# Kernel tuning notes

Hardware: AMD Instinct MI355X
Metric: run time of the kernel (lower is better)

Reference implementation:

```python
import jax, jax.numpy as jnp
import numpy as np

N_QUBITS = 8
N_CYCLES = 4
N_LAYERS = 2  # log2(8) - 1
B = 65536

CNOT = jnp.array([[1, 0, 0, 0],
                  [0, 1, 0, 0],
                  [0, 0, 0, 1],
                  [0, 0, 1, 0]], dtype=jnp.complex64)


def apply_gate(state, U, wires):
    """Apply a (2^k x 2^k) gate U on the given wires of state (B, 2,2,...,2).
    Wire 0 is the leftmost (most significant) qubit axis."""
    k = len(wires)
    src = [w + 1 for w in wires]
    dst = list(range(1, 1 + k))
    st = jnp.moveaxis(state, src, dst)
    shp = st.shape
    st = st.reshape(shp[0], 2 ** k, -1)
    st = jnp.einsum('ij,bjr->bir', U, st)
    return jnp.moveaxis(st.reshape(shp), dst, src)


def apply_ry(state, q, angles):
    """Batched RY(angle) on qubit q; angles has shape (B,)."""
    st = jnp.moveaxis(state, q + 1, 1)  # (B, 2, rest...)
    c = jnp.cos(0.5 * angles).reshape((-1,) + (1,) * (st.ndim - 2))
    s = jnp.sin(0.5 * angles).reshape((-1,) + (1,) * (st.ndim - 2))
    s0, s1 = st[:, 0], st[:, 1]
    new = jnp.stack([c * s0 - s * s1, s * s0 + c * s1], axis=1)
    return jnp.moveaxis(new, 1, q + 1)


def crx_mat(theta):
    c = (jnp.cos(0.5 * theta) + 0j).astype(jnp.complex64)
    s = (-1j * jnp.sin(0.5 * theta)).astype(jnp.complex64)
    one = jnp.ones((), jnp.complex64)
    zero = jnp.zeros((), jnp.complex64)
    return jnp.stack([
        jnp.stack([one, zero, zero, zero]),
        jnp.stack([zero, one, zero, zero]),
        jnp.stack([zero, zero, c, s]),
        jnp.stack([zero, zero, s, c]),
    ])


def u3_mat(p):
    th, ph, lm = p[0], p[1], p[2]
    ct = (jnp.cos(0.5 * th) + 0j).astype(jnp.complex64)
    st = (jnp.sin(0.5 * th) + 0j).astype(jnp.complex64)
    el = jnp.exp(1j * lm).astype(jnp.complex64)
    ep = jnp.exp(1j * ph).astype(jnp.complex64)
    return jnp.stack([
        jnp.stack([ct, -el * st]),
        jnp.stack([ep * st, ep * el * ct]),
    ])


def expval_z(state, q):
    st = jnp.moveaxis(state, q + 1, 1)
    p = (st.real ** 2 + st.imag ** 2).reshape(st.shape[0], 2, -1).sum(-1)
    return p[:, 0] - p[:, 1]


def _forward(x, crx_theta, u3_params, w1, b1, w2, b2):
    b = x.shape[0]
    # |0...0> initial state, shape (B, 2,2,...,2)
    state = jnp.zeros((b, 2 ** N_QUBITS), jnp.complex64).at[:, 0].set(1.0)
    state = state.reshape((b,) + (2,) * N_QUBITS)
    # encoder: data re-uploading RY angle encoding + CNOT ring, n_cycles times
    for _ in range(N_CYCLES):
        for q in range(N_QUBITS):
            state = apply_ry(state, q, x[:, q])
        for q in range(N_QUBITS):
            state = apply_gate(state, CNOT, [q, (q + 1) % N_QUBITS])
    # QCNN conv/pool layers with shared weights per layer
    active = list(range(N_QUBITS))
    for layer in range(N_LAYERS):
        U = crx_mat(crx_theta[layer])
        for i in range(0, len(active) - 1, 2):
            state = apply_gate(state, U, [active[i], active[i + 1]])
        for i in range(1, len(active) - 1, 2):
            state = apply_gate(state, U, [active[i], active[i + 1]])
        remain = active[1::2]
        # mid-circuit expval in the original is discarded and does not alter state
        V = u3_mat(u3_params[layer])
        for q in remain:
            state = apply_gate(state, V, [q])
        active = remain
    feats = jnp.stack([expval_z(state, q) for q in active], axis=1)  # (B, 2)
    h = jnp.tanh(feats @ w1 + b1)
    return jax.nn.sigmoid(h @ w2 + b2)  # (B, 1)


def setup_inputs() -> dict:
    key = jax.random.key(0)
    ks = jax.random.split(key, 6)
    return {
        'x': jax.random.normal(ks[0], (B, N_QUBITS), jnp.float32),
        'crx_theta': jax.random.normal(ks[1], (N_LAYERS,), jnp.float32),
        'u3_params': jax.random.normal(ks[2], (N_LAYERS, 3), jnp.float32),
        'w1': jax.random.normal(ks[3], (2, 10), jnp.float32) * 0.5,
        'b1': jnp.zeros((10,), jnp.float32),
        'w2': jax.random.normal(ks[4], (10, 1), jnp.float32) * 0.5,
        'b2': jnp.zeros((1,), jnp.float32),
    }


def reference(x, crx_theta, u3_params, w1, b1, w2, b2):
    return _forward(x, crx_theta, u3_params, w1, b1, w2, b2)
```

## Files before the change

### kernel.cpp

```cpp
#include <hip/hip_runtime.h>


#define NQ 8

typedef float v2 __attribute__((ext_vector_type(2)));

__device__ __forceinline__ v2 sp(float x) { return (v2){x, x}; }
__device__ __forceinline__ v2 fma2(v2 a, v2 b, v2 c) { return __builtin_elementwise_fma(a, b, c); }
__device__ __forceinline__ v2 swp(v2 v) { return __builtin_shufflevector(v, v, 1, 0); }

template<int M>
__device__ __forceinline__ float sx(float v) {
    if constexpr (M == 32) return __shfl_xor(v, 32, 64);
    else return __int_as_float(__builtin_amdgcn_ds_swizzle(
                 __float_as_int(v), (M << 10) | 0x1F));
}
template<int M>
__device__ __forceinline__ v2 sx2(v2 v) {
    v2 r; r.x = sx<M>(v.x); r.y = sx<M>(v.y); return r;
}
__device__ __forceinline__ float bperm(int byte_addr, float v) {
    return __int_as_float(__builtin_amdgcn_ds_bpermute(byte_addr, __float_as_int(v)));
}

#define RY_L(q, M) do { \
    v2 oA = sx2<M>(A), oB = sx2<M>(B); \
    A = fma2(sp(c[q]), A, sp(ts[q]) * oA); \
    B = fma2(sp(c[q]), B, sp(ts[q]) * oB); \
} while(0)

#define CNOT_FUSED() do { \
    v2 TA = pb ? B : A; \
    v2 TS = pb ? A : B; \
    A = (v2){ bperm(ba0, TA.x), bperm(ba1, TA.y) }; \
    B = (v2){ bperm(ba0, TS.y), bperm(ba1, TS.x) }; \
} while(0)

#define CRX_LL(CSH, M, cc, sn) do { \
    const bool ct = (l >> (CSH)) & 1; \
    v2 oRa = sx2<M>(Ra), oIa = sx2<M>(Ia), oRb = sx2<M>(Rb), oIb = sx2<M>(Ib); \
    if (ct) { \
        Ra = fma2(sp(cc), Ra, sp(sn)  * oIa); \
        Ia = fma2(sp(cc), Ia, sp(-(sn)) * oRa); \
        Rb = fma2(sp(cc), Rb, sp(sn)  * oIb); \
        Ib = fma2(sp(cc), Ib, sp(-(sn)) * oRb); \
    } \
} while(0)

#define RYC0(M, T) do { \
    v2 oRa = sx2<M>(Ra), oIa = sx2<M>(Ia), oRb = sx2<M>(Rb), oIb = sx2<M>(Ib); \
    Ra = fma2(sp(uct0), Ra, sp(T) * oRa); Ia = fma2(sp(uct0), Ia, sp(T) * oIa); \
    Rb = fma2(sp(uct0), Rb, sp(T) * oRb); Ib = fma2(sp(uct0), Ib, sp(T) * oIb); \
} while(0)

__global__ void qcnn_prep(const float* __restrict__ crx,
                          const float* __restrict__ u3p,
                          float* __restrict__ ws) {
    if (threadIdx.x == 0 && blockIdx.x == 0) {
        float sc0, cc0, sc1, cc1;
        __sincosf(0.5f * crx[0], &sc0, &cc0);
        __sincosf(0.5f * crx[1], &sc1, &cc1);
        ws[0] = cc0; ws[1] = sc0; ws[2] = cc1; ws[3] = sc1;
        float lm0, ph0;
        {
            float th = u3p[0]; ph0 = u3p[1]; lm0 = u3p[2];
            float st_, ct_;
            __sincosf(0.5f * th, &st_, &ct_);
            ws[4] = ct_; ws[5] = st_;
        }
        {
            float th = u3p[3], ph = u3p[4], lm = u3p[5];
            float st_, ct_, sl, cl, sp_, cp, spl, cpl;
            __sincosf(0.5f * th, &st_, &ct_);
            __sincosf(lm, &sl, &cl);
            __sincosf(ph, &sp_, &cp);
            __sincosf(ph + lm, &spl, &cpl);
            ws[8] = ct_;  ws[9] = st_;  ws[10] = cl; ws[11] = sl; ws[12] = cp; ws[13] = sp_;
            ws[14] = -st_ * cl;  ws[15] = -st_ * sl;
            ws[16] =  st_ * cp;  ws[17] =  st_ * sp_;
            ws[18] =  ct_ * cpl; ws[19] =  ct_ * spl;
        }
        for (int k = 0; k < 4; ++k) {
            float kf = (float)k;
            float sA0, cA0, sB0, cB0, sA1, cA1, sB1, cB1;
            __sincosf(kf * lm0,         &sA0, &cA0);
            __sincosf((kf + 1.f) * lm0, &sB0, &cB0);
            __sincosf(kf * ph0,         &sA1, &cA1);
            __sincosf((kf + 1.f) * ph0, &sB1, &cB1);
            float* q = ws + 20 + k * 8;
            q[0] = cA0; q[1] = sA0; q[2] = cB0; q[3] = sB0;
            q[4] = cA1; q[5] = sA1; q[6] = cB1; q[7] = sB1;
        }
    }
}

__global__ __launch_bounds__(256) void qcnn_kernel(
    const float* __restrict__ x,
    const float* __restrict__ ws,
    const float* __restrict__ w1,
    const float* __restrict__ b1,
    const float* __restrict__ w2,
    const float* __restrict__ b2,
    float* __restrict__ out,
    int Btot)
{
    const int gtid = blockIdx.x * blockDim.x + threadIdx.x;
    const int wave = gtid >> 6;
    const int l = threadIdx.x & 63;
    if (wave >= Btot) return;

    const bool pb = __builtin_popcount(l) & 1;
    const int addr0 = (l & 32) | ((l ^ (l >> 1)) & 31);
    const int ba0 = addr0 << 2;
    const int ba1 = ba0 ^ (48 << 2);

    const float4* xv = (const float4*)(x + wave * NQ);
    float4 xa = xv[0], xb = xv[1];
    float c[NQ], s[NQ], ts[6];
    {
        float ang[NQ] = {xa.x, xa.y, xa.z, xa.w, xb.x, xb.y, xb.z, xb.w};
#pragma unroll
        for (int q = 0; q < NQ; ++q) __sincosf(0.5f * ang[q], &s[q], &c[q]);
#pragma unroll
        for (int q = 0; q < 6; ++q) ts[q] = ((l >> (5 - q)) & 1) ? s[q] : -s[q];
    }

    const float crc0 = ws[0], crs0 = ws[1], crc1 = ws[2], crs1 = ws[3];
    const float uct0 = ws[4], ust0 = ws[5];
    const float uct1 = ws[8],  ust1 = ws[9],  cl1 = ws[10], sl1 = ws[11], cp1 = ws[12], sp1 = ws[13];
    const float u01r1 = ws[14], u01i1 = ws[15], u10r1 = ws[16], u10i1 = ws[17], u11r1 = ws[18], u11i1 = ws[19];

    const int ki = ((l >> 4) & 1) + ((l >> 2) & 1) + (l & 1);
    const float4* dtab = (const float4*)(ws + 20 + ki * 8);
    float4 d0 = dtab[0], d1 = dtab[1];
    const v2 CAB_lm = {d0.x, d0.z}, SAB_lm = {d0.y, d0.w};
    const v2 CAB_ph = {d1.x, d1.z}, SAB_ph = {d1.y, d1.w};
    const float tu1 = ((l >> 4) & 1) ? ust0 : -ust0;
    const float tu3 = ((l >> 2) & 1) ? ust0 : -ust0;
    const float tu5 = (l & 1)        ? ust0 : -ust0;

    v2 A, B;
    {
        float pl = (((l >> 5) & 1) ? s[0] : c[0]);
        pl *= (((l >> 4) & 1) ? s[1] : c[1]);
        pl *= (((l >> 3) & 1) ? s[2] : c[2]);
        pl *= (((l >> 2) & 1) ? s[3] : c[3]);
        pl *= (((l >> 1) & 1) ? s[4] : c[4]);
        pl *= ((l & 1) ? s[5] : c[5]);
        v2 cs7 = {c[7], s[7]};
        A = sp(pl * c[6]) * cs7;
        B = sp(pl * s[6]) * cs7;
    }
    CNOT_FUSED();
#pragma unroll
    for (int cyc = 0; cyc < 3; ++cyc) {
        RY_L(0, 32); RY_L(1, 16); RY_L(2, 8); RY_L(3, 4); RY_L(4, 2); RY_L(5, 1);
        {
            v2 nA = fma2(sp(-s[6]), B, sp(c[6]) * A);
            B = fma2(sp(c[6]), B, sp(s[6]) * A);
            A = nA;
        }
        {
            v2 sv = {-s[7], s[7]};
            A = fma2(sp(c[7]), A, sv * swp(A));
            B = fma2(sp(c[7]), B, sv * swp(B));
        }
        CNOT_FUSED();
    }

    v2 Ra = A, Rb = B, Ia = sp(0.f), Ib = sp(0.f);

    {
        const bool ct = (l >> 5) & 1;
        v2 oRa = sx2<16>(Ra), oRb = sx2<16>(Rb);
        if (ct) {
            Ia = sp(-crs0) * oRa; Ra = sp(crc0) * Ra;
            Ib = sp(-crs0) * oRb; Rb = sp(crc0) * Rb;
        }
    }
    CRX_LL(3, 4, crc0, crs0);
    CRX_LL(1, 1, crc0, crs0);
    {
        v2 nRb = fma2(sp(crc0), Rb, sp(crs0) * swp(Ib));
        Ib = fma2(sp(crc0), Ib, sp(-crs0) * swp(Rb));
        Rb = nRb;
    }
    CRX_LL(4, 8, crc0, crs0);
    CRX_LL(2, 2, crc0, crs0);
    {
        if (l & 1) {
            v2 nRa = fma2(sp(crc0), Ra, sp(crs0) * Ib);
            v2 nRb = fma2(sp(crc0), Rb, sp(crs0) * Ia);
            v2 nIa = fma2(sp(crc0), Ia, sp(-crs0) * Rb);
            v2 nIb = fma2(sp(crc0), Ib, sp(-crs0) * Ra);
            Ra = nRa; Rb = nRb; Ia = nIa; Ib = nIb;
        }
    }
    {
        v2 nRa = fma2(CAB_lm, Ra, -SAB_lm * Ia);
        Ia = fma2(CAB_lm, Ia, SAB_lm * Ra); Ra = nRa;
        v2 nRb = fma2(CAB_lm, Rb, -SAB_lm * Ib);
        Ib = fma2(CAB_lm, Ib, SAB_lm * Rb); Rb = nRb;
    }
    RYC0(16, tu1);
    RYC0(4,  tu3);
    RYC0(1,  tu5);
    {
        v2 usv = {-ust0, ust0};
        Ra = fma2(sp(uct0), Ra, usv * swp(Ra));
        Rb = fma2(sp(uct0), Rb, usv * swp(Rb));
        Ia = fma2(sp(uct0), Ia, usv * swp(Ia));
        Ib = fma2(sp(uct0), Ib, usv * swp(Ib));
    }
    {
        v2 nRa = fma2(CAB_ph, Ra, -SAB_ph * Ia);
        Ia = fma2(CAB_ph, Ia, SAB_ph * Ra); Ra = nRa;
        v2 nRb = fma2(CAB_ph, Rb, -SAB_ph * Ib);
        Ib = fma2(CAB_ph, Ib, SAB_ph * Rb); Rb = nRb;
    }

    CRX_LL(4, 4, crc1, crs1);
    {
        if (l & 1) {
            v2 nRa = fma2(sp(crc1), Ra, sp(crs1) * swp(Ia));
            v2 nIa = fma2(sp(crc1), Ia, sp(-crs1) * swp(Ra));
            v2 nRb = fma2(sp(crc1), Rb, sp(crs1) * swp(Ib));
            v2 nIb = fma2(sp(crc1), Ib, sp(-crs1) * swp(Rb));
            Ra = nRa; Ia = nIa; Rb = nRb; Ib = nIb;
        }
    }
    CRX_LL(2, 1, crc1, crs1);
    {
        const bool b = (l >> 2) & 1;
        if (b) {
            v2 nRa = fma2(sp(cl1), Ra, sp(-sl1) * Ia);
            Ia = fma2(sp(cl1), Ia, sp(sl1) * Ra); Ra = nRa;
            v2 nRb = fma2(sp(cl1), Rb, sp(-sl1) * Ib);
            Ib = fma2(sp(cl1), Ib, sp(sl1) * Rb); Rb = nRb;
        }
        const float t = b ? ust1 : -ust1;
        v2 oRa = sx2<4>(Ra), oIa = sx2<4>(Ia), oRb = sx2<4>(Rb), oIb = sx2<4>(Ib);
        Ra = fma2(sp(uct1), Ra, sp(t) * oRa); Ia = fma2(sp(uct1), Ia, sp(t) * oIa);
        Rb = fma2(sp(uct1), Rb, sp(t) * oRb); Ib = fma2(sp(uct1), Ib, sp(t) * oIb);
        if (b) {
            v2 nRa = fma2(sp(cp1), Ra, sp(-sp1) * Ia);
            Ia = fma2(sp(cp1), Ia, sp(sp1) * Ra); Ra = nRa;
            v2 nRb = fma2(sp(cp1), Rb, sp(-sp1) * Ib);
            Ib = fma2(sp(cp1), Ib, sp(sp1) * Rb); Rb = nRb;
        }
    }
    {
        v2 E0 = {uct1, u11r1}, E1 = {u01r1, u10r1};
        v2 E2 = {0.f, -u11i1}, E3 = {-u01i1, -u10i1};
        v2 G2 = {0.f,  u11i1}, G3 = { u01i1,  u10i1};
        v2 sRa = swp(Ra), sIa = swp(Ia), sRb = swp(Rb), sIb = swp(Ib);
        v2 nRa = fma2(E3, sIa, fma2(E2, Ia, fma2(E1, sRa, E0 * Ra)));
        v2 nIa = fma2(G3, sRa, fma2(G2, Ra, fma2(E1, sIa, E0 * Ia)));
        v2 nRb = fma2(E3, sIb, fma2(E2, Ib, fma2(E1, sRb, E0 * Rb)));
        v2 nIb = fma2(G3, sRb, fma2(G2, Rb, fma2(E1, sIb, E0 * Ib)));
        Ra = nRa; Ia = nIa; Rb = nRb; Ib = nIb;
    }

    v2 Na = fma2(Ia, Ia, Ra * Ra);
    v2 Nb = fma2(Ib, Ib, Rb * Rb);
    v2 T = Na + Nb;
    const float sgn = ((l >> 2) & 1) ? -1.0f : 1.0f;
    v2 F = { sgn * (T.x + T.y), T.x - T.y };
    F += sx2<1>(F);
    F += sx2<2>(F);
    F += sx2<4>(F);
    F += sx2<8>(F);
    F += sx2<16>(F);
    F += sx2<32>(F);

    const int k = l & 15;
    float contrib = 0.0f;
    if (k < 10) {
        float z = fmaf(F.x, w1[k], fmaf(F.y, w1[10 + k], b1[k]));
        float e = __expf(2.0f * z);
        float h = (e - 1.0f) / (e + 1.0f);
        contrib = h * w2[k];
    }
    contrib += sx<1>(contrib);
    contrib += sx<2>(contrib);
    contrib += sx<4>(contrib);
    contrib += sx<8>(contrib);
    if (l == 0) {
        float a = contrib + b2[0];
        out[wave] = 1.0f / (1.0f + __expf(-a));
    }
}

extern "C" void kernel_launch(void* const* d_in, const int* in_sizes, int n_in,
                              void* d_out, int out_size, void* d_ws, size_t ws_size,
                              hipStream_t stream) {
    const float* x   = (const float*)d_in[0];
    const float* crx = (const float*)d_in[1];
    const float* u3p = (const float*)d_in[2];
    const float* w1  = (const float*)d_in[3];
    const float* b1  = (const float*)d_in[4];
    const float* w2  = (const float*)d_in[5];
    const float* b2  = (const float*)d_in[6];
    float* out = (float*)d_out;
    float* ws  = (float*)d_ws;

    const int B = in_sizes[0] / NQ;
    hipLaunchKernelGGL(qcnn_prep, dim3(1), dim3(64), 0, stream, crx, u3p, ws);
    const int wavesPerBlock = 256 / 64;
    const int grid = (B + wavesPerBlock - 1) / wavesPerBlock;
    hipLaunchKernelGGL(qcnn_kernel, dim3(grid), dim3(256), 0, stream,
                       x, ws, w1, b1, w2, b2, out, B);
}
```

Baseline: 128.6 us.

## Map 8 batch elements per wave with 32 amplitudes per lane in registers

Restructures the state-vector mapping so each wave simulates 8 circuits (8 lanes per circuit, 32 amplitudes per lane as 16 v2 registers) instead of one circuit spread across 64 lanes. Most gates on high qubits become in-register arithmetic and register renaming rather than cross-lane swizzles or bpermutes, and lane exchanges use DPP moves. The separate prep kernel is removed, with each lane recomputing the gate trig constants. In exchange, register pressure rises sharply and per-lane redundant sincos work is added, which may lower occupancy.

Result: slower. 467.1 us (+263.4%).

```diff
diff --git a/kernel.cpp b/kernel.cpp
--- a/kernel.cpp
+++ b/kernel.cpp
@@ -9,94 +9,24 @@
 __device__ __forceinline__ v2 fma2(v2 a, v2 b, v2 c) { return __builtin_elementwise_fma(a, b, c); }
 __device__ __forceinline__ v2 swp(v2 v) { return __builtin_shufflevector(v, v, 1, 0); }
 
+template<int CTRL>
+__device__ __forceinline__ float dppf(float v) {
+    return __int_as_float(__builtin_amdgcn_mov_dpp(__float_as_int(v), CTRL, 0xF, 0xF, true));
+}
 template<int M>
 __device__ __forceinline__ float sx(float v) {
-    if constexpr (M == 32) return __shfl_xor(v, 32, 64);
+    if constexpr (M == 1)      return dppf<0xB1>(v);
+    else if constexpr (M == 2) return dppf<0x4E>(v);
     else return __int_as_float(__builtin_amdgcn_ds_swizzle(
-                 __float_as_int(v), (M << 10) | 0x1F));
+                __float_as_int(v), (M << 10) | 0x1F));
 }
 template<int M>
-__device__ __forceinline__ v2 sx2(v2 v) {
-    v2 r; r.x = sx<M>(v.x); r.y = sx<M>(v.y); return r;
-}
-__device__ __forceinline__ float bperm(int byte_addr, float v) {
-    return __int_as_float(__builtin_amdgcn_ds_bpermute(byte_addr, __float_as_int(v)));
-}
-
-#define RY_L(q, M) do { \
-    v2 oA = sx2<M>(A), oB = sx2<M>(B); \
-    A = fma2(sp(c[q]), A, sp(ts[q]) * oA); \
-    B = fma2(sp(c[q]), B, sp(ts[q]) * oB); \
-} while(0)
-
-#define CNOT_FUSED() do { \
-    v2 TA = pb ? B : A; \
-    v2 TS = pb ? A : B; \
-    A = (v2){ bperm(ba0, TA.x), bperm(ba1, TA.y) }; \
-    B = (v2){ bperm(ba0, TS.y), bperm(ba1, TS.x) }; \
-} while(0)
-
-#define CRX_LL(CSH, M, cc, sn) do { \
-    const bool ct = (l >> (CSH)) & 1; \
-    v2 oRa = sx2<M>(Ra), oIa = sx2<M>(Ia), oRb = sx2<M>(Rb), oIb = sx2<M>(Ib); \
-    if (ct) { \
-        Ra = fma2(sp(cc), Ra, sp(sn)  * oIa); \
-        Ia = fma2(sp(cc), Ia, sp(-(sn)) * oRa); \
-        Rb = fma2(sp(cc), Rb, sp(sn)  * oIb); \
-        Ib = fma2(sp(cc), Ib, sp(-(sn)) * oRb); \
-    } \
-} while(0)
-
-#define RYC0(M, T) do { \
-    v2 oRa = sx2<M>(Ra), oIa = sx2<M>(Ia), oRb = sx2<M>(Rb), oIb = sx2<M>(Ib); \
-    Ra = fma2(sp(uct0), Ra, sp(T) * oRa); Ia = fma2(sp(uct0), Ia, sp(T) * oIa); \
-    Rb = fma2(sp(uct0), Rb, sp(T) * oRb); Ib = fma2(sp(uct0), Ib, sp(T) * oIb); \
-} while(0)
-
-__global__ void qcnn_prep(const float* __restrict__ crx,
-                          const float* __restrict__ u3p,
-                          float* __restrict__ ws) {
-    if (threadIdx.x == 0 && blockIdx.x == 0) {
-        float sc0, cc0, sc1, cc1;
-        __sincosf(0.5f * crx[0], &sc0, &cc0);
-        __sincosf(0.5f * crx[1], &sc1, &cc1);
-        ws[0] = cc0; ws[1] = sc0; ws[2] = cc1; ws[3] = sc1;
-        float lm0, ph0;
-        {
-            float th = u3p[0]; ph0 = u3p[1]; lm0 = u3p[2];
-            float st_, ct_;
-            __sincosf(0.5f * th, &st_, &ct_);
-            ws[4] = ct_; ws[5] = st_;
-        }
-        {
-            float th = u3p[3], ph = u3p[4], lm = u3p[5];
-            float st_, ct_, sl, cl, sp_, cp, spl, cpl;
-            __sincosf(0.5f * th, &st_, &ct_);
-            __sincosf(lm, &sl, &cl);
-            __sincosf(ph, &sp_, &cp);
-            __sincosf(ph + lm, &spl, &cpl);
-            ws[8] = ct_;  ws[9] = st_;  ws[10] = cl; ws[11] = sl; ws[12] = cp; ws[13] = sp_;
-            ws[14] = -st_ * cl;  ws[15] = -st_ * sl;
-            ws[16] =  st_ * cp;  ws[17] =  st_ * sp_;
-            ws[18] =  ct_ * cpl; ws[19] =  ct_ * spl;
-        }
-        for (int k = 0; k < 4; ++k) {
-            float kf = (float)k;
-            float sA0, cA0, sB0, cB0, sA1, cA1, sB1, cB1;
-            __sincosf(kf * lm0,         &sA0, &cA0);
-            __sincosf((kf + 1.f) * lm0, &sB0, &cB0);
-            __sincosf(kf * ph0,         &sA1, &cA1);
-            __sincosf((kf + 1.f) * ph0, &sB1, &cB1);
-            float* q = ws + 20 + k * 8;
-            q[0] = cA0; q[1] = sA0; q[2] = cB0; q[3] = sB0;
-            q[4] = cA1; q[5] = sA1; q[6] = cB1; q[7] = sB1;
-        }
-    }
-}
+__device__ __forceinline__ v2 sx2(v2 v) { v2 r; r.x = sx<M>(v.x); r.y = sx<M>(v.y); return r; }
 
 __global__ __launch_bounds__(256) void qcnn_kernel(
     const float* __restrict__ x,
-    const float* __restrict__ ws,
+    const float* __restrict__ crx,
+    const float* __restrict__ u3p,
     const float* __restrict__ w1,
     const float* __restrict__ b1,
     const float* __restrict__ w2,
@@ -105,189 +35,261 @@
     int Btot)
 {
     const int gtid = blockIdx.x * blockDim.x + threadIdx.x;
-    const int wave = gtid >> 6;
+    const int wv = gtid >> 6;
     const int l = threadIdx.x & 63;
-    if (wave >= Btot) return;
-
-    const bool pb = __builtin_popcount(l) & 1;
-    const int addr0 = (l & 32) | ((l ^ (l >> 1)) & 31);
-    const int ba0 = addr0 << 2;
-    const int ba1 = ba0 ^ (48 << 2);
-
-    const float4* xv = (const float4*)(x + wave * NQ);
+    const int e = wv * 8 + (l >> 3);
+    const int p = l & 7;
+    const bool p2 = (p >> 2) & 1, p1b = (p >> 1) & 1, p0 = p & 1;
+    if (e >= Btot) return;
+
+    const float4* xv = (const float4*)(x + e * NQ);
     float4 xa = xv[0], xb = xv[1];
-    float c[NQ], s[NQ], ts[6];
-    {
-        float ang[NQ] = {xa.x, xa.y, xa.z, xa.w, xb.x, xb.y, xb.z, xb.w};
-#pragma unroll
-        for (int q = 0; q < NQ; ++q) __sincosf(0.5f * ang[q], &s[q], &c[q]);
-#pragma unroll
-        for (int q = 0; q < 6; ++q) ts[q] = ((l >> (5 - q)) & 1) ? s[q] : -s[q];
-    }
-
-    const float crc0 = ws[0], crs0 = ws[1], crc1 = ws[2], crs1 = ws[3];
-    const float uct0 = ws[4], ust0 = ws[5];
-    const float uct1 = ws[8],  ust1 = ws[9],  cl1 = ws[10], sl1 = ws[11], cp1 = ws[12], sp1 = ws[13];
-    const float u01r1 = ws[14], u01i1 = ws[15], u10r1 = ws[16], u10i1 = ws[17], u11r1 = ws[18], u11i1 = ws[19];
-
-    const int ki = ((l >> 4) & 1) + ((l >> 2) & 1) + (l & 1);
-    const float4* dtab = (const float4*)(ws + 20 + ki * 8);
-    float4 d0 = dtab[0], d1 = dtab[1];
-    const v2 CAB_lm = {d0.x, d0.z}, SAB_lm = {d0.y, d0.w};
-    const v2 CAB_ph = {d1.x, d1.z}, SAB_ph = {d1.y, d1.w};
-    const float tu1 = ((l >> 4) & 1) ? ust0 : -ust0;
-    const float tu3 = ((l >> 2) & 1) ? ust0 : -ust0;
-    const float tu5 = (l & 1)        ? ust0 : -ust0;
-
-    v2 A, B;
-    {
-        float pl = (((l >> 5) & 1) ? s[0] : c[0]);
-        pl *= (((l >> 4) & 1) ? s[1] : c[1]);
-        pl *= (((l >> 3) & 1) ? s[2] : c[2]);
-        pl *= (((l >> 2) & 1) ? s[3] : c[3]);
-        pl *= (((l >> 1) & 1) ? s[4] : c[4]);
-        pl *= ((l & 1) ? s[5] : c[5]);
-        v2 cs7 = {c[7], s[7]};
-        A = sp(pl * c[6]) * cs7;
-        B = sp(pl * s[6]) * cs7;
-    }
-    CNOT_FUSED();
+    float ang[NQ] = {xa.x, xa.y, xa.z, xa.w, xb.x, xb.y, xb.z, xb.w};
+    float cq[NQ], sq[NQ];
+#pragma unroll
+    for (int q = 0; q < NQ; ++q) __sincosf(0.5f * ang[q], &sq[q], &cq[q]);
+    const float t0 = p2  ? sq[0] : -sq[0];
+    const float t1 = p1b ? sq[1] : -sq[1];
+    const float t2 = p0  ? sq[2] : -sq[2];
+
+    float sn0, cc0, sn1, cc1;
+    __sincosf(0.5f * crx[0], &sn0, &cc0);
+    __sincosf(0.5f * crx[1], &sn1, &cc1);
+    const float th0 = u3p[0], ph0 = u3p[1], lm0 = u3p[2];
+    float ust0, uct0; __sincosf(0.5f * th0, &ust0, &uct0);
+    const float p1f = p1b ? 1.0f : 0.0f;
+    float clm[4], slm[4], cph[4], sph[4];
+#pragma unroll
+    for (int j = 0; j < 4; ++j) __sincosf(lm0 * (p1f + (float)j), &slm[j], &clm[j]);
+#pragma unroll
+    for (int j = 0; j < 4; ++j) __sincosf(ph0 * (p1f + (float)j), &sph[j], &cph[j]);
+    const float th1 = u3p[3], ph1 = u3p[4], lm1 = u3p[5];
+    float ust1, uct1; __sincosf(0.5f * th1, &ust1, &uct1);
+    float sl1, cl1;   __sincosf(lm1, &sl1, &cl1);
+    float sp1, cp1;   __sincosf(ph1, &sp1, &cp1);
+    const float cpl1 = cp1 * cl1 - sp1 * sl1, spl1 = sp1 * cl1 + cp1 * sl1;
+    const float u01r1 = -ust1 * cl1, u01i1 = -ust1 * sl1;
+    const float u10r1 =  ust1 * cp1, u10i1 =  ust1 * sp1;
+    const float u11r1 =  uct1 * cpl1, u11i1 = uct1 * spl1;
+
+    v2 A[16];
+    {
+        float P4[4], P8[8], P16[16];
+        float P2[2] = {cq[3], sq[3]};
+#pragma unroll
+        for (int j = 0; j < 4; ++j)  P4[j]  = P2[j >> 1] * ((j & 1) ? sq[4] : cq[4]);
+#pragma unroll
+        for (int j = 0; j < 8; ++j)  P8[j]  = P4[j >> 1] * ((j & 1) ? sq[5] : cq[5]);
+#pragma unroll
+        for (int j = 0; j < 16; ++j) P16[j] = P8[j >> 1] * ((j & 1) ? sq[6] : cq[6]);
+        float fl = (p2 ? sq[0] : cq[0]) * (p1b ? sq[1] : cq[1]) * (p0 ? sq[2] : cq[2]);
+        v2 fv = sp(fl) * (v2){cq[7], sq[7]};
+#pragma unroll
+        for (int i = 0; i < 16; ++i) A[i] = sp(P16[i]) * fv;
+    }
+
+#define CNOT_RING_R() do { \
+    { _Pragma("unroll") for (int i = 0; i < 16; ++i) { v2 o = sx2<2>(A[i]); A[i] = p2 ? o : A[i]; } } \
+    { _Pragma("unroll") for (int i = 0; i < 16; ++i) { v2 o = sx2<1>(A[i]); A[i] = p1b ? o : A[i]; } } \
+    { v2 T[16]; _Pragma("unroll") for (int i = 0; i < 16; ++i) T[i] = A[i]; \
+      _Pragma("unroll") for (int i = 0; i < 16; ++i) A[i] = p0 ? T[i ^ 8] : T[i]; } \
+    { _Pragma("unroll") for (int u = 8; u < 12; ++u) { v2 t = A[u]; A[u] = A[u + 4]; A[u + 4] = t; } } \
+    { _Pragma("unroll") for (int u = 0; u < 16; ++u) if ((u & 4) && !(u & 2)) { v2 t = A[u]; A[u] = A[u + 2]; A[u + 2] = t; } } \
+    { _Pragma("unroll") for (int u = 0; u < 16; ++u) if ((u & 2) && !(u & 1)) { v2 t = A[u]; A[u] = A[u + 1]; A[u + 1] = t; } } \
+    { _Pragma("unroll") for (int i = 1; i < 16; i += 2) A[i] = swp(A[i]); } \
+    { _Pragma("unroll") for (int i = 0; i < 16; ++i) A[i].y = sx<4>(A[i].y); } \
+} while (0)
+
+    CNOT_RING_R();
 #pragma unroll
     for (int cyc = 0; cyc < 3; ++cyc) {
-        RY_L(0, 32); RY_L(1, 16); RY_L(2, 8); RY_L(3, 4); RY_L(4, 2); RY_L(5, 1);
-        {
-            v2 nA = fma2(sp(-s[6]), B, sp(c[6]) * A);
-            B = fma2(sp(c[6]), B, sp(s[6]) * A);
-            A = nA;
-        }
-        {
-            v2 sv = {-s[7], s[7]};
-            A = fma2(sp(c[7]), A, sv * swp(A));
-            B = fma2(sp(c[7]), B, sv * swp(B));
-        }
-        CNOT_FUSED();
-    }
-
-    v2 Ra = A, Rb = B, Ia = sp(0.f), Ib = sp(0.f);
-
-    {
-        const bool ct = (l >> 5) & 1;
-        v2 oRa = sx2<16>(Ra), oRb = sx2<16>(Rb);
-        if (ct) {
-            Ia = sp(-crs0) * oRa; Ra = sp(crc0) * Ra;
-            Ib = sp(-crs0) * oRb; Rb = sp(crc0) * Rb;
-        }
-    }
-    CRX_LL(3, 4, crc0, crs0);
-    CRX_LL(1, 1, crc0, crs0);
-    {
-        v2 nRb = fma2(sp(crc0), Rb, sp(crs0) * swp(Ib));
-        Ib = fma2(sp(crc0), Ib, sp(-crs0) * swp(Rb));
-        Rb = nRb;
-    }
-    CRX_LL(4, 8, crc0, crs0);
-    CRX_LL(2, 2, crc0, crs0);
-    {
-        if (l & 1) {
-            v2 nRa = fma2(sp(crc0), Ra, sp(crs0) * Ib);
-            v2 nRb = fma2(sp(crc0), Rb, sp(crs0) * Ia);
-            v2 nIa = fma2(sp(crc0), Ia, sp(-crs0) * Rb);
-            v2 nIb = fma2(sp(crc0), Ib, sp(-crs0) * Ra);
-            Ra = nRa; Rb = nRb; Ia = nIa; Ib = nIb;
-        }
-    }
-    {
-        v2 nRa = fma2(CAB_lm, Ra, -SAB_lm * Ia);
-        Ia = fma2(CAB_lm, Ia, SAB_lm * Ra); Ra = nRa;
-        v2 nRb = fma2(CAB_lm, Rb, -SAB_lm * Ib);
-        Ib = fma2(CAB_lm, Ib, SAB_lm * Rb); Rb = nRb;
-    }
-    RYC0(16, tu1);
-    RYC0(4,  tu3);
-    RYC0(1,  tu5);
+        { _Pragma("unroll") for (int i = 0; i < 16; ++i) { v2 o = sx2<4>(A[i]); A[i] = fma2(sp(cq[0]), A[i], sp(t0) * o); } }
+        { _Pragma("unroll") for (int i = 0; i < 16; ++i) { v2 o = sx2<2>(A[i]); A[i] = fma2(sp(cq[1]), A[i], sp(t1) * o); } }
+        { _Pragma("unroll") for (int i = 0; i < 16; ++i) { v2 o = sx2<1>(A[i]); A[i] = fma2(sp(cq[2]), A[i], sp(t2) * o); } }
+        { _Pragma("unroll") for (int u = 0; u < 8; ++u) {
+            v2 a0 = A[u], a1 = A[u + 8];
+            A[u]     = fma2(sp(cq[3]), a0, sp(-sq[3]) * a1);
+            A[u + 8] = fma2(sp(sq[3]), a0, sp(cq[3]) * a1); } }
+        { _Pragma("unroll") for (int u = 0; u < 16; ++u) if (!(u & 4)) {
+            v2 a0 = A[u], a1 = A[u + 4];
+            A[u]     = fma2(sp(cq[4]), a0, sp(-sq[4]) * a1);
+            A[u + 4] = fma2(sp(sq[4]), a0, sp(cq[4]) * a1); } }
+        { _Pragma("unroll") for (int u = 0; u < 16; ++u) if (!(u & 2)) {
+            v2 a0 = A[u], a1 = A[u + 2];
+            A[u]     = fma2(sp(cq[5]), a0, sp(-sq[5]) * a1);
+            A[u + 2] = fma2(sp(sq[5]), a0, sp(cq[5]) * a1); } }
+        { _Pragma("unroll") for (int u = 0; u < 16; u += 2) {
+            v2 a0 = A[u], a1 = A[u + 1];
+            A[u]     = fma2(sp(cq[6]), a0, sp(-sq[6]) * a1);
+            A[u + 1] = fma2(sp(sq[6]), a0, sp(cq[6]) * a1); } }
+        { v2 sv = {-sq[7], sq[7]};
+          _Pragma("unroll") for (int i = 0; i < 16; ++i)
+            A[i] = fma2(sp(cq[7]), A[i], sv * swp(A[i])); }
+        CNOT_RING_R();
+    }
+
+    v2 Re[16], Im[16];
+#pragma unroll
+    for (int i = 0; i < 16; ++i) { Re[i] = A[i]; Im[i] = sp(0.f); }
+
+#define CRX_PAIR(u, v, cc, sn) { \
+    v2 nRu = fma2(sp(cc), Re[u], sp(sn) * Im[v]); \
+    v2 nIu = fma2(sp(cc), Im[u], sp(-(sn)) * Re[v]); \
+    v2 nRv = fma2(sp(cc), Re[v], sp(sn) * Im[u]); \
+    v2 nIv = fma2(sp(cc), Im[v], sp(-(sn)) * Re[u]); \
+    Re[u] = nRu; Im[u] = nIu; Re[v] = nRv; Im[v] = nIv; }
+
+#define CMUL(u, C, S) { \
+    v2 nR_ = fma2(C, Re[u], -(S) * Im[u]); \
+    Im[u] = fma2(C, Im[u], (S) * Re[u]); \
+    Re[u] = nR_; }
+
+    {
+        _Pragma("unroll") for (int i = 0; i < 16; ++i) {
+            v2 o = sx2<2>(Re[i]);
+            if (p2) { Im[i] = sp(-sn0) * o; Re[i] = sp(cc0) * Re[i]; }
+        }
+    }
+    if (p0) {
+        _Pragma("unroll") for (int u = 0; u < 8; ++u) CRX_PAIR(u, u + 8, cc0, sn0);
+    }
+    {
+        _Pragma("unroll") for (int u = 0; u < 16; ++u) if ((u & 4) && !(u & 2)) CRX_PAIR(u, u + 2, cc0, sn0);
+    }
+    {
+        _Pragma("unroll") for (int i = 1; i < 16; i += 2) {
+            v2 nR = fma2(sp(cc0), Re[i], sp(sn0) * swp(Im[i]));
+            v2 nI = fma2(sp(cc0), Im[i], sp(-sn0) * swp(Re[i]));
+            Re[i] = nR; Im[i] = nI;
+        }
+    }
+    {
+        _Pragma("unroll") for (int i = 0; i < 16; ++i) {
+            v2 oR = sx2<1>(Re[i]), oI = sx2<1>(Im[i]);
+            if (p1b) {
+                Re[i] = fma2(sp(cc0), Re[i], sp(sn0) * oI);
+                Im[i] = fma2(sp(cc0), Im[i], sp(-sn0) * oR);
+            }
+        }
+    }
+    {
+        _Pragma("unroll") for (int u = 8; u < 12; ++u) CRX_PAIR(u, u + 4, cc0, sn0);
+    }
+    {
+        _Pragma("unroll") for (int u = 0; u < 16; ++u) if ((u & 2) && !(u & 1)) CRX_PAIR(u, u + 1, cc0, sn0);
+    }
+
+    {
+        _Pragma("unroll") for (int i = 0; i < 16; ++i) {
+            const int bi = (i >> 3) + ((i >> 1) & 1);
+            v2 C = {clm[bi], clm[bi + 1]}, S = {slm[bi], slm[bi + 1]};
+            CMUL(i, C, S);
+        }
+    }
+    {
+        const float tu = p1b ? ust0 : -ust0;
+        _Pragma("unroll") for (int i = 0; i < 16; ++i) {
+            v2 oR = sx2<2>(Re[i]), oI = sx2<2>(Im[i]);
+            Re[i] = fma2(sp(uct0), Re[i], sp(tu) * oR);
+            Im[i] = fma2(sp(uct0), Im[i], sp(tu) * oI);
+        }
+    }
+    {
+        _Pragma("unroll") for (int u = 0; u < 8; ++u) {
+            v2 r0 = Re[u], r1 = Re[u + 8], i0 = Im[u], i1 = Im[u + 8];
+            Re[u]     = fma2(sp(uct0), r0, sp(-ust0) * r1);
+            Re[u + 8] = fma2(sp(ust0), r0, sp(uct0) * r1);
+            Im[u]     = fma2(sp(uct0), i0, sp(-ust0) * i1);
+            Im[u + 8] = fma2(sp(ust0), i0, sp(uct0) * i1);
+        }
+    }
+    {
+        _Pragma("unroll") for (int u = 0; u < 16; ++u) if (!(u & 2)) {
+            v2 r0 = Re[u], r1 = Re[u + 2], i0 = Im[u], i1 = Im[u + 2];
+            Re[u]     = fma2(sp(uct0), r0, sp(-ust0) * r1);
+            Re[u + 2] = fma2(sp(ust0), r0, sp(uct0) * r1);
+            Im[u]     = fma2(sp(uct0), i0, sp(-ust0) * i1);
+            Im[u + 2] = fma2(sp(ust0), i0, sp(uct0) * i1);
+        }
+    }
     {
         v2 usv = {-ust0, ust0};
-        Ra = fma2(sp(uct0), Ra, usv * swp(Ra));
-        Rb = fma2(sp(uct0), Rb, usv * swp(Rb));
-        Ia = fma2(sp(uct0), Ia, usv * swp(Ia));
-        Ib = fma2(sp(uct0), Ib, usv * swp(Ib));
-    }
-    {
-        v2 nRa = fma2(CAB_ph, Ra, -SAB_ph * Ia);
-        Ia = fma2(CAB_ph, Ia, SAB_ph * Ra); Ra = nRa;
-        v2 nRb = fma2(CAB_ph, Rb, -SAB_ph * Ib);
-        Ib = fma2(CAB_ph, Ib, SAB_ph * Rb); Rb = nRb;
-    }
-
-    CRX_LL(4, 4, crc1, crs1);
-    {
-        if (l & 1) {
-            v2 nRa = fma2(sp(crc1), Ra, sp(crs1) * swp(Ia));
-            v2 nIa = fma2(sp(crc1), Ia, sp(-crs1) * swp(Ra));
-            v2 nRb = fma2(sp(crc1), Rb, sp(crs1) * swp(Ib));
-            v2 nIb = fma2(sp(crc1), Ib, sp(-crs1) * swp(Rb));
-            Ra = nRa; Ia = nIa; Rb = nRb; Ib = nIb;
-        }
-    }
-    CRX_LL(2, 1, crc1, crs1);
-    {
-        const bool b = (l >> 2) & 1;
-        if (b) {
-            v2 nRa = fma2(sp(cl1), Ra, sp(-sl1) * Ia);
-            Ia = fma2(sp(cl1), Ia, sp(sl1) * Ra); Ra = nRa;
-            v2 nRb = fma2(sp(cl1), Rb, sp(-sl1) * Ib);
-            Ib = fma2(sp(cl1), Ib, sp(sl1) * Rb); Rb = nRb;
-        }
-        const float t = b ? ust1 : -ust1;
-        v2 oRa = sx2<4>(Ra), oIa = sx2<4>(Ia), oRb = sx2<4>(Rb), oIb = sx2<4>(Ib);
-        Ra = fma2(sp(uct1), Ra, sp(t) * oRa); Ia = fma2(sp(uct1), Ia, sp(t) * oIa);
-        Rb = fma2(sp(uct1), Rb, sp(t) * oRb); Ib = fma2(sp(uct1), Ib, sp(t) * oIb);
-        if (b) {
-            v2 nRa = fma2(sp(cp1), Ra, sp(-sp1) * Ia);
-            Ia = fma2(sp(cp1), Ia, sp(sp1) * Ra); Ra = nRa;
-            v2 nRb = fma2(sp(cp1), Rb, sp(-sp1) * Ib);
-            Ib = fma2(sp(cp1), Ib, sp(sp1) * Rb); Rb = nRb;
-        }
+        _Pragma("unroll") for (int i = 0; i < 16; ++i) {
+            Re[i] = fma2(sp(uct0), Re[i], usv * swp(Re[i]));
+            Im[i] = fma2(sp(uct0), Im[i], usv * swp(Im[i]));
+        }
+    }
+    {
+        _Pragma("unroll") for (int i = 0; i < 16; ++i) {
+            const int bi = (i >> 3) + ((i >> 1) & 1);
+            v2 C = {cph[bi], cph[bi + 1]}, S = {sph[bi], sph[bi + 1]};
+            CMUL(i, C, S);
+        }
+    }
+
+    if (p1b) {
+        _Pragma("unroll") for (int u = 0; u < 8; ++u) CRX_PAIR(u, u + 8, cc1, sn1);
+    }
+    {
+        _Pragma("unroll") for (int i = 0; i < 16; ++i) if ((i >> 1) & 1) {
+            v2 nR = fma2(sp(cc1), Re[i], sp(sn1) * swp(Im[i]));
+            v2 nI = fma2(sp(cc1), Im[i], sp(-sn1) * swp(Re[i]));
+            Re[i] = nR; Im[i] = nI;
+        }
+    }
+    {
+        _Pragma("unroll") for (int u = 8; u < 16; ++u) if (!(u & 2)) CRX_PAIR(u, u + 2, cc1, sn1);
+    }
+    {
+        _Pragma("unroll") for (int u = 8; u < 16; ++u) CMUL(u, sp(cl1), sp(sl1));
+        _Pragma("unroll") for (int u = 0; u < 8; ++u) {
+            v2 r0 = Re[u], r1 = Re[u + 8], i0 = Im[u], i1 = Im[u + 8];
+            Re[u]     = fma2(sp(uct1), r0, sp(-ust1) * r1);
+            Re[u + 8] = fma2(sp(ust1), r0, sp(uct1) * r1);
+            Im[u]     = fma2(sp(uct1), i0, sp(-ust1) * i1);
+            Im[u + 8] = fma2(sp(ust1), i0, sp(uct1) * i1);
+        }
+        _Pragma("unroll") for (int u = 8; u < 16; ++u) CMUL(u, sp(cp1), sp(sp1));
     }
     {
         v2 E0 = {uct1, u11r1}, E1 = {u01r1, u10r1};
         v2 E2 = {0.f, -u11i1}, E3 = {-u01i1, -u10i1};
         v2 G2 = {0.f,  u11i1}, G3 = { u01i1,  u10i1};
-        v2 sRa = swp(Ra), sIa = swp(Ia), sRb = swp(Rb), sIb = swp(Ib);
-        v2 nRa = fma2(E3, sIa, fma2(E2, Ia, fma2(E1, sRa, E0 * Ra)));
-        v2 nIa = fma2(G3, sRa, fma2(G2, Ra, fma2(E1, sIa, E0 * Ia)));
-        v2 nRb = fma2(E3, sIb, fma2(E2, Ib, fma2(E1, sRb, E0 * Rb)));
-        v2 nIb = fma2(G3, sRb, fma2(G2, Rb, fma2(E1, sIb, E0 * Ib)));
-        Ra = nRa; Ia = nIa; Rb = nRb; Ib = nIb;
-    }
-
-    v2 Na = fma2(Ia, Ia, Ra * Ra);
-    v2 Nb = fma2(Ib, Ib, Rb * Rb);
-    v2 T = Na + Nb;
-    const float sgn = ((l >> 2) & 1) ? -1.0f : 1.0f;
-    v2 F = { sgn * (T.x + T.y), T.x - T.y };
+        _Pragma("unroll") for (int i = 0; i < 16; ++i) {
+            v2 sR = swp(Re[i]), sI = swp(Im[i]);
+            v2 nR = fma2(E3, sI, fma2(E2, Im[i], fma2(E1, sR, E0 * Re[i])));
+            v2 nI = fma2(G3, sR, fma2(G2, Re[i], fma2(E1, sI, E0 * Im[i])));
+            Re[i] = nR; Im[i] = nI;
+        }
+    }
+
+    v2 Spos = sp(0.f), Sneg = sp(0.f);
+#pragma unroll
+    for (int i = 0; i < 8; ++i)  Spos += fma2(Im[i], Im[i], Re[i] * Re[i]);
+#pragma unroll
+    for (int i = 8; i < 16; ++i) Sneg += fma2(Im[i], Im[i], Re[i] * Re[i]);
+    float f3 = (Spos.x + Spos.y) - (Sneg.x + Sneg.y);
+    v2 S = Spos + Sneg;
+    float f7 = S.x - S.y;
+    v2 F = {f3, f7};
     F += sx2<1>(F);
     F += sx2<2>(F);
     F += sx2<4>(F);
-    F += sx2<8>(F);
-    F += sx2<16>(F);
-    F += sx2<32>(F);
-
-    const int k = l & 15;
-    float contrib = 0.0f;
-    if (k < 10) {
-        float z = fmaf(F.x, w1[k], fmaf(F.y, w1[10 + k], b1[k]));
-        float e = __expf(2.0f * z);
-        float h = (e - 1.0f) / (e + 1.0f);
-        contrib = h * w2[k];
-    }
-    contrib += sx<1>(contrib);
-    contrib += sx<2>(contrib);
-    contrib += sx<4>(contrib);
-    contrib += sx<8>(contrib);
-    if (l == 0) {
-        float a = contrib + b2[0];
-        out[wave] = 1.0f / (1.0f + __expf(-a));
+
+    float z1 = fmaf(F.x, w1[p], fmaf(F.y, w1[10 + p], b1[p]));
+    float e1 = __expf(2.0f * z1);
+    float acc = ((e1 - 1.0f) / (e1 + 1.0f)) * w2[p];
+    if (p < 2) {
+        float z2 = fmaf(F.x, w1[p + 8], fmaf(F.y, w1[18 + p], b1[p + 8]));
+        float e2 = __expf(2.0f * z2);
+        acc = fmaf((e2 - 1.0f) / (e2 + 1.0f), w2[p + 8], acc);
+    }
+    acc += sx<1>(acc);
+    acc += sx<2>(acc);
+    acc += sx<4>(acc);
+    if (p == 0) {
+        float a = acc + b2[0];
+        out[e] = 1.0f / (1.0f + __expf(-a));
     }
 }
 
@@ -302,12 +304,11 @@
     const float* w2  = (const float*)d_in[5];
     const float* b2  = (const float*)d_in[6];
     float* out = (float*)d_out;
-    float* ws  = (float*)d_ws;
 
     const int B = in_sizes[0] / NQ;
-    hipLaunchKernelGGL(qcnn_prep, dim3(1), dim3(64), 0, stream, crx, u3p, ws);
+    const int waves = (B + 7) / 8;
     const int wavesPerBlock = 256 / 64;
-    const int grid = (B + wavesPerBlock - 1) / wavesPerBlock;
+    const int grid = (waves + wavesPerBlock - 1) / wavesPerBlock;
     hipLaunchKernelGGL(qcnn_kernel, dim3(grid), dim3(256), 0, stream,
-                       x, ws, w1, b1, w2, b2, out, B);
+                       x, crx, u3p, w1, b1, w2, b2, out, B);
 }
```
